# Optimization experiments

Hardware: AMD Instinct MI355X
Metric: run time of the kernel (lower is better)

## Reference

```python
import jax, jax.numpy as jnp
import numpy as np

N_NODES = 50000


def _pointnet_layer(h, pos, src, dst, wA, bA, wB, bB):
    # message: MLP(concat(h_j, pos_j - pos_i)) per edge, then max-aggregate at dst
    m = jnp.concatenate([h[src], pos[src] - pos[dst]], axis=-1)  # [E, in+3]
    m = jax.nn.relu(m @ wA + bA) @ wB + bB                       # [E, out]
    agg = jax.ops.segment_max(m, dst, num_segments=N_NODES)     # [N, out]
    # PyG max-aggregation returns 0 for nodes with no incoming edges
    return jnp.where(jnp.isfinite(agg), agg, 0.0)


def setup_inputs() -> dict:
    key = jax.random.key(0)
    ks = jax.random.split(key, 16)
    num_points, num_features, E = 256, 256, 800000
    s = 0.05
    inp = {
        "x": jax.random.normal(ks[0], (N_NODES, num_points), dtype=jnp.float32),
        "pos": jax.random.normal(ks[1], (N_NODES, 3), dtype=jnp.float32),
        "edge_index": jax.random.randint(ks[2], (2, E), 0, N_NODES, dtype=jnp.int64),
        # conv1 mlp: (num_points+3 -> F -> F)
        "w1a": jax.random.normal(ks[3], (num_points + 3, num_features), dtype=jnp.float32) * s,
        "b1a": jnp.zeros((num_features,), dtype=jnp.float32),
        "w1b": jax.random.normal(ks[4], (num_features, num_features), dtype=jnp.float32) * s,
        "b1b": jnp.zeros((num_features,), dtype=jnp.float32),
        # conv2 mlp: (F+3 -> F -> F)
        "w2a": jax.random.normal(ks[5], (num_features + 3, num_features), dtype=jnp.float32) * s,
        "b2a": jnp.zeros((num_features,), dtype=jnp.float32),
        "w2b": jax.random.normal(ks[6], (num_features, num_features), dtype=jnp.float32) * s,
        "b2b": jnp.zeros((num_features,), dtype=jnp.float32),
        # decoder: F -> 256 -> num_points
        "wd1": jax.random.normal(ks[7], (num_features, 256), dtype=jnp.float32) * s,
        "bd1": jnp.zeros((256,), dtype=jnp.float32),
        "wd2": jax.random.normal(ks[8], (256, num_points), dtype=jnp.float32) * s,
        "bd2": jnp.zeros((num_points,), dtype=jnp.float32),
    }
    return inp


def reference(x, pos, edge_index, w1a, b1a, w1b, b1b, w2a, b2a, w2b, b2b, wd1, bd1, wd2, bd2):
    src, dst = edge_index[0], edge_index[1]  # message flows j(src) -> i(dst)
    h = jax.nn.relu(_pointnet_layer(x, pos, src, dst, w1a, b1a, w1b, b1b))
    h = jax.nn.relu(_pointnet_layer(h, pos, src, dst, w2a, b2a, w2b, b2b))
    decoded = jax.nn.relu(h @ wd1 + bd1) @ wd2 + bd2  # [N, num_points]
    return decoded
```

## Files before the change

kernel.cpp:

```cpp
#include <hip/hip_runtime.h>
#include <stdint.h>


using bf16x8 = __attribute__((ext_vector_type(8))) short;
using f32x4  = __attribute__((ext_vector_type(4))) float;

#define AB_STRIDE 40
#define ABUF      2560
#define ZSTRIDE   68

#define BARRIER_NOVM() asm volatile("s_waitcnt lgkmcnt(0)\n\ts_barrier" ::: "memory")

__device__ __forceinline__ float b2f(uint32_t v16) {
    return __uint_as_float(v16 << 16);
}
__device__ __forceinline__ float b2f_hi(uint32_t w) {
    return __uint_as_float(w & 0xffff0000u);
}
__device__ __forceinline__ uint16_t f2b(float f) {
    uint32_t u = __float_as_uint(f);
    u += 0x7fffu + ((u >> 16) & 1u);
    return (uint16_t)(u >> 16);
}
#if __has_builtin(__builtin_amdgcn_cvt_pk_bf16_f32)
__device__ __forceinline__ uint32_t pack2bf(float lo, float hi) {
    auto r = __builtin_amdgcn_cvt_pk_bf16_f32(lo, hi);
    uint32_t u; __builtin_memcpy(&u, &r, 4); return u;
}
#else
__device__ __forceinline__ uint32_t pack2bf(float lo, float hi) {
    return (uint32_t)f2b(lo) | ((uint32_t)f2b(hi) << 16);
}
#endif
__device__ __forceinline__ uint32_t encf(float f) {
    uint32_t u = __float_as_uint(f);
    return (u & 0x80000000u) ? ~u : (u | 0x80000000u);
}
__device__ __forceinline__ float decf(uint32_t k) {
    uint32_t u = (k & 0x80000000u) ? (k & 0x7fffffffu) : ~k;
    return __uint_as_float(u);
}

__global__ void detect_fmt(const uint32_t* __restrict__ x,
                           const uint32_t* __restrict__ ei,
                           uint32_t* __restrict__ flags) {
    if (threadIdx.x == 0 && blockIdx.x == 0) {
        int plaus = 0;
        for (int i = 0; i < 64; i++) {
            uint32_t v = x[i];
            uint32_t e = (v >> 23) & 0xffu;
            if (v == 0u || (e >= 96u && e <= 150u)) plaus++;
        }
        flags[0] = (plaus >= 48) ? 1u : 0u;
        int zeros = 0;
        for (int i = 0; i < 16; i++)
            if (ei[2 * i + 1] == 0u) zeros++;
        flags[1] = (zeros == 16) ? 1u : 0u;
    }
}

struct ConvArgs {
    const void* src[13];
    uint32_t dstOff[13];
    uint32_t n[13];
};

__global__ __launch_bounds__(256) void convert_small(
        ConvArgs a, uint16_t* __restrict__ dstBase, const uint32_t* __restrict__ flags) {
    bool isf32 = flags[0] != 0u;
    int t = blockIdx.y;
    int i = blockIdx.x * 256 + threadIdx.x;
    if (i >= (int)a.n[t]) return;
    uint16_t* d = dstBase + a.dstOff[t];
    d[i] = isf32 ? f2b(((const float*)a.src[t])[i]) : ((const uint16_t*)a.src[t])[i];
}

__global__ __launch_bounds__(256) void init_hist_agg(
        uint32_t* __restrict__ agg, int n4, int* __restrict__ hist, int N) {
    int i = blockIdx.x * 256 + threadIdx.x;
    if (i < n4) {
        uint4 v = {0x80000000u, 0x80000000u, 0x80000000u, 0x80000000u};
        ((uint4*)agg)[i] = v;
    }
    int i4 = i * 4;
    if (i4 + 3 < N) {
        uint4 z = {0, 0, 0, 0};
        ((uint4*)hist)[i] = z;
    } else if (i4 < N) {
        for (int j = i4; j < N; j++) hist[j] = 0;
    }
}

__global__ __launch_bounds__(256) void hist_dst(
        const int* __restrict__ ei_raw, int E, int* __restrict__ hist,
        const uint32_t* __restrict__ flags) {
    bool i64 = flags[1] != 0u;
    int e = blockIdx.x * 256 + threadIdx.x;
    if (e < E) {
        int d = i64 ? ei_raw[2 * (E + e)] : ei_raw[E + e];
        atomicAdd(&hist[d], 1);
    }
}

__global__ __launch_bounds__(1024) void scan_partial(
        const int* __restrict__ hist, int* __restrict__ cursor,
        int* __restrict__ part, int N) {
    __shared__ int wsum[16];
    int tid = threadIdx.x, lane = tid & 63, wid = tid >> 6;
    int base = blockIdx.x * 1024;
    int v = (base + tid < N) ? hist[base + tid] : 0;
    int x = v;
#pragma unroll
    for (int s = 1; s < 64; s <<= 1) {
        int t = __shfl_up(x, s, 64);
        if (lane >= s) x += t;
    }
    if (lane == 63) wsum[wid] = x;
    __syncthreads();
    if (wid == 0 && lane < 16) {
        int w = wsum[lane];
#pragma unroll
        for (int s = 1; s < 16; s <<= 1) {
            int t = __shfl_up(w, s, 64);
            if (lane >= s) w += t;
        }
        wsum[lane] = w;
    }
    __syncthreads();
    int wbase = (wid > 0) ? wsum[wid - 1] : 0;
    if (base + tid < N) cursor[base + tid] = x - v + wbase;
    if (tid == 0) part[blockIdx.x] = wsum[15];
}

__global__ __launch_bounds__(1024) void scan_carry(
        const int* __restrict__ part, int* __restrict__ carry, int B) {
    __shared__ int wsum[16];
    int tid = threadIdx.x, lane = tid & 63, wid = tid >> 6;
    int v = (tid < B) ? part[tid] : 0;
    int x = v;
#pragma unroll
    for (int s = 1; s < 64; s <<= 1) {
        int t = __shfl_up(x, s, 64);
        if (lane >= s) x += t;
    }
    if (lane == 63) wsum[wid] = x;
    __syncthreads();
    if (wid == 0 && lane < 16) {
        int w = wsum[lane];
#pragma unroll
        for (int s = 1; s < 16; s <<= 1) {
            int t = __shfl_up(w, s, 64);
            if (lane >= s) w += t;
        }
        wsum[lane] = w;
    }
    __syncthreads();
    int wbase = (wid > 0) ? wsum[wid - 1] : 0;
    if (tid < B) carry[tid] = x - v + wbase;
}

__global__ __launch_bounds__(1024) void scan_add(
        int* __restrict__ cursor, const int* __restrict__ carry, int N) {
    int i = blockIdx.x * 1024 + threadIdx.x;
    if (i < N) cursor[i] += carry[blockIdx.x];
}

__global__ __launch_bounds__(256) void scatter_edges(
        const int* __restrict__ ei_raw, int E, int* __restrict__ cursor,
        int* __restrict__ esrc, int* __restrict__ edst,
        const uint32_t* __restrict__ flags) {
    bool i64 = flags[1] != 0u;
    int e = blockIdx.x * 256 + threadIdx.x;
    if (e < E) {
        int s = i64 ? ei_raw[2 * e] : ei_raw[e];
        int d = i64 ? ei_raw[2 * (E + e)] : ei_raw[E + e];
        int p = atomicAdd(&cursor[d], 1);
        esrc[p] = s;
        edst[p] = d;
    }
}

__global__ __launch_bounds__(256) void transpose_w(
        const uint16_t* s0, const uint16_t* s1, const uint16_t* s2,
        const uint16_t* s3, const uint16_t* s4, const uint16_t* s5,
        uint16_t* dst) {
    const uint16_t* srcs[6] = {s0, s1, s2, s3, s4, s5};
    const uint16_t* src = srcs[blockIdx.y];
    uint16_t* d = dst + (size_t)blockIdx.y * 65536;
    int k = blockIdx.x;
    int n = threadIdx.x;
    d[(k >> 5) * 8192 + n * 32 + (k & 31)] = src[k * 256 + n];
}

__global__ __launch_bounds__(256) void pos_proj(
        const uint16_t* pos, const uint16_t* wpos, uint16_t* Q, int N) {
    int t = threadIdx.x;
    int r = t >> 5, c8 = (t & 31) * 8;
    int i = blockIdx.x * 8 + r;
    if (i >= N) return;
    uint4 wv0 = *(const uint4*)(wpos + c8);
    uint4 wv1 = *(const uint4*)(wpos + 256 + c8);
    uint4 wv2 = *(const uint4*)(wpos + 512 + c8);
    float p0 = b2f(pos[i * 3 + 0]);
    float p1 = b2f(pos[i * 3 + 1]);
    float p2 = b2f(pos[i * 3 + 2]);
    uint32_t w0[4] = {wv0.x, wv0.y, wv0.z, wv0.w};
    uint32_t w1[4] = {wv1.x, wv1.y, wv1.z, wv1.w};
    uint32_t w2[4] = {wv2.x, wv2.y, wv2.z, wv2.w};
    uint32_t o[4];
#pragma unroll
    for (int j = 0; j < 4; j++) {
        float lo = p0 * b2f(w0[j] & 0xffffu) + p1 * b2f(w1[j] & 0xffffu) + p2 * b2f(w2[j] & 0xffffu);
        float hi = p0 * b2f_hi(w0[j]) + p1 * b2f_hi(w1[j]) + p2 * b2f_hi(w2[j]);
        o[j] = pack2bf(lo, hi);
    }
    uint4 ov = {o[0], o[1], o[2], o[3]};
    *(uint4*)(Q + (size_t)i * 256 + c8) = ov;
}

template <int AMODE, int OUTMODE, int REINIT>
__global__ __launch_bounds__(256, 3) void gemm_node(
        const void* __restrict__ Araw, const uint16_t* __restrict__ BT,
        const uint16_t* __restrict__ bias, const uint16_t* __restrict__ Qadd,
        void* __restrict__ out, int M, const uint32_t* __restrict__ flags,
        uint32_t* __restrict__ aggwb) {
    __shared__ __align__(16) uint16_t Al[2 * 64 * AB_STRIDE];
    int tid = threadIdx.x;
    int tileM = blockIdx.x;
    int wave = tid >> 6, lane = tid & 63, lrow = lane & 15, quad = lane >> 4;
    int row = tid >> 2, kq = (tid & 3) * 8;
    f32x4 acc[4][4] = {};

    int rg = tileM * 64 + row;
    bool rok = rg < M;
    int rgc = rok ? rg : (M - 1);
    bool isf32 = false;
    if (AMODE == 2 || OUTMODE == 2) isf32 = flags[0] != 0u;

    const uint16_t* a16 = (const uint16_t*)Araw + (size_t)rgc * 256 + kq;
    const uint32_t* a32 = (const uint32_t*)Araw + (size_t)rgc * 256 + kq;
    const uint16_t* bfrag = BT + (wave * 64 + lrow) * 32 + quad * 8;
    uint16_t* awr = Al + row * AB_STRIDE + kq;
    const uint16_t* ard = Al + lrow * AB_STRIDE + quad * 8;

    uint4 p0 = {0, 0, 0, 0}, p1 = {0, 0, 0, 0};
    if (AMODE == 0) {
        p0 = *(const uint4*)a16;
    } else if (AMODE == 1) {
        p0 = *(const uint4*)a32; p1 = *(const uint4*)(a32 + 4);
    } else {
        if (isf32) { p0 = *(const uint4*)a32; p1 = *(const uint4*)(a32 + 4); }
        else       { p0 = *(const uint4*)a16; }
    }

#pragma unroll
    for (int kc = 0; kc < 256; kc += 32) {
        int buf = (kc >> 5) & 1;
        uint4 wv;
        if (AMODE == 0 || (AMODE == 2 && !isf32)) {
            wv = p0;
        } else if (AMODE == 1) {
            uint32_t a[8] = {p0.x, p0.y, p0.z, p0.w, p1.x, p1.y, p1.z, p1.w};
            wv.x = pack2bf(decf(a[0]), decf(a[1]));
            wv.y = pack2bf(decf(a[2]), decf(a[3]));
            wv.z = pack2bf(decf(a[4]), decf(a[5]));
            wv.w = pack2bf(decf(a[6]), decf(a[7]));
        } else {
            wv.x = pack2bf(__uint_as_float(p0.x), __uint_as_float(p0.y));
            wv.y = pack2bf(__uint_as_float(p0.z), __uint_as_float(p0.w));
            wv.z = pack2bf(__uint_as_float(p1.x), __uint_as_float(p1.y));
            wv.w = pack2bf(__uint_as_float(p1.z), __uint_as_float(p1.w));
        }
        *(uint4*)(awr + buf * ABUF) = wv;
        const uint16_t* bp = bfrag + (kc >> 5) * 8192;
        bf16x8 bfv[4];
#pragma unroll
        for (int c = 0; c < 4; c++) bfv[c] = *(const bf16x8*)(bp + c * 512);
        if (kc < 224) {
            if (AMODE == 0) {
                p0 = *(const uint4*)(a16 + kc + 32);
            } else if (AMODE == 1) {
                p0 = *(const uint4*)(a32 + kc + 32);
                p1 = *(const uint4*)(a32 + kc + 36);
            } else {
                if (isf32) { p0 = *(const uint4*)(a32 + kc + 32);
                             p1 = *(const uint4*)(a32 + kc + 36); }
                else       { p0 = *(const uint4*)(a16 + kc + 32); }
            }
        }
        BARRIER_NOVM();
        const uint16_t* ar = ard + buf * ABUF;
        bf16x8 af[4];
#pragma unroll
        for (int r = 0; r < 4; r++) af[r] = *(const bf16x8*)(ar + r * 16 * AB_STRIDE);
#pragma unroll
        for (int r = 0; r < 4; r++)
#pragma unroll
            for (int c = 0; c < 4; c++)
                acc[r][c] = __builtin_amdgcn_mfma_f32_16x16x32_bf16(af[r], bfv[c], acc[r][c], 0, 0, 0);
    }

    if (AMODE == 1 && REINIT && rok) {
        uint32_t* wb = aggwb + (size_t)rg * 256 + kq;
        uint4 z = {0x80000000u, 0x80000000u, 0x80000000u, 0x80000000u};
#pragma unroll
        for (int kc = 0; kc < 256; kc += 32) {
            *(uint4*)(wb + kc) = z;
            *(uint4*)(wb + kc + 4) = z;
        }
    }

#pragma unroll
    for (int c = 0; c < 4; c++) {
        int col = wave * 64 + c * 16 + lrow;
        float bv = b2f(bias[col]);
#pragma unroll
        for (int r = 0; r < 4; r++) {
#pragma unroll
            for (int i = 0; i < 4; i++) {
                int rw = tileM * 64 + r * 16 + quad * 4 + i;
                if (rw >= M) continue;
                float v = acc[r][c][i] + bv;
                if (OUTMODE == 0) {
                    v += b2f(Qadd[(size_t)rw * 256 + col]);
                    ((uint16_t*)out)[(size_t)rw * 256 + col] = f2b(v);
                } else if (OUTMODE == 1) {
                    v = fmaxf(v, 0.f);
                    ((uint16_t*)out)[(size_t)rw * 256 + col] = f2b(v);
                } else {
                    if (isf32) ((float*)out)[(size_t)rw * 256 + col] = v;
                    else       ((uint16_t*)out)[(size_t)rw * 256 + col] = f2b(v);
                }
            }
        }
    }
}

__global__ __launch_bounds__(256, 3) void edge_gemm_agg(
        const uint16_t* __restrict__ Gs16, const uint16_t* __restrict__ Qb,
        const uint16_t* __restrict__ BT, const uint16_t* __restrict__ bias,
        const int* __restrict__ esrc, const int* __restrict__ edst, int E,
        uint32_t* __restrict__ agg) {
    __shared__ __align__(16) uint16_t SM[256 * ZSTRIDE];
    uint16_t* Al = SM;
    uint16_t* Zl = SM;
    __shared__ int sdst[64];
    __shared__ uint64_t smask;
    int tid = threadIdx.x;
    int ebase = blockIdx.x * 64;
    int evalid = (E - ebase < 64) ? (E - ebase) : 64;
    if (tid < 64) sdst[tid] = (tid < evalid) ? edst[ebase + tid] : 0;

    int wave = tid >> 6, lane = tid & 63, lrow = lane & 15, quad = lane >> 4;
    int row = tid >> 2, kq = (tid & 3) * 8;
    int er = (row < evalid) ? row : (evalid - 1);
    int s = esrc[ebase + er];
    int d = edst[ebase + er];
    const uint16_t* gbase = Gs16 + (size_t)s * 256 + kq;
    const uint16_t* qbase = Qb   + (size_t)d * 256 + kq;
    const uint16_t* bfrag = BT + (wave * 64 + lrow) * 32 + quad * 8;
    uint16_t* awr = Al + row * AB_STRIDE + kq;
    const uint16_t* ard = Al + lrow * AB_STRIDE + quad * 8;

    f32x4 acc[4][4] = {};
    uint4 g = *(const uint4*)gbase;
    uint4 q = *(const uint4*)qbase;

#pragma unroll
    for (int kc = 0; kc < 256; kc += 32) {
        int buf = (kc >> 5) & 1;
        uint32_t gw[4] = {g.x, g.y, g.z, g.w};
        uint32_t qw[4] = {q.x, q.y, q.z, q.w};
        uint32_t mw[4];
#pragma unroll
        for (int j = 0; j < 4; j++) {
            float lo = fmaxf(b2f(gw[j] & 0xffffu) - b2f(qw[j] & 0xffffu), 0.f);
            float hi = fmaxf(b2f_hi(gw[j]) - b2f_hi(qw[j]), 0.f);
            mw[j] = pack2bf(lo, hi);
        }
        uint4 wv = {mw[0], mw[1], mw[2], mw[3]};
        *(uint4*)(awr + buf * ABUF) = wv;
        const uint16_t* bp = bfrag + (kc >> 5) * 8192;
        bf16x8 bfv[4];
#pragma unroll
        for (int c = 0; c < 4; c++) bfv[c] = *(const bf16x8*)(bp + c * 512);
        if (kc < 224) {
            g = *(const uint4*)(gbase + kc + 32);
            q = *(const uint4*)(qbase + kc + 32);
        }
        BARRIER_NOVM();
        const uint16_t* ar = ard + buf * ABUF;
        bf16x8 af[4];
#pragma unroll
        for (int r = 0; r < 4; r++) af[r] = *(const bf16x8*)(ar + r * 16 * AB_STRIDE);
#pragma unroll
        for (int r = 0; r < 4; r++)
#pragma unroll
            for (int c = 0; c < 4; c++)
                acc[r][c] = __builtin_amdgcn_mfma_f32_16x16x32_bf16(af[r], bfv[c], acc[r][c], 0, 0, 0);
    }
    __syncthreads();

    float bv[4];
#pragma unroll
    for (int c = 0; c < 4; c++) bv[c] = b2f(bias[wave * 64 + c * 16 + lrow]);
#pragma unroll
    for (int c = 0; c < 4; c++) {
        int col = wave * 64 + c * 16 + lrow;
#pragma unroll
        for (int r = 0; r < 4; r++) {
            uint2 z4 = {pack2bf(acc[r][c][0] + bv[c], acc[r][c][1] + bv[c]),
                        pack2bf(acc[r][c][2] + bv[c], acc[r][c][3] + bv[c])};
            *(uint2*)&Zl[col * ZSTRIDE + r * 16 + quad * 4] = z4;
        }
    }
    if (wave == 0) {
        int d0 = sdst[lane];
        int dp = (lane > 0) ? sdst[lane - 1] : -1;
        uint64_t m = __ballot(d0 != dp);
        if (lane == 0) smask = m;
    }
    __syncthreads();

    uint64_t mask = smask;
    int col = tid;
    const uint16_t* zc = &Zl[col * ZSTRIDE];
    float run = 0.f;
#pragma unroll 4
    for (int gi = 0; gi < 16; gi++) {
        int rbase = gi * 4;
        if (rbase >= evalid) break;
        uint2 z4 = *(const uint2*)&zc[rbase];
        float vv[4] = {b2f(z4.x & 0xffffu), b2f_hi(z4.x),
                       b2f(z4.y & 0xffffu), b2f_hi(z4.y)};
#pragma unroll
        for (int i = 0; i < 4; i++) {
            int r = rbase + i;
            if (r >= evalid) break;
            if (r == 0) {
                run = vv[0];
            } else if ((mask >> r) & 1ull) {
                int dp = sdst[r - 1];
                atomicMax(agg + (size_t)dp * 256 + col, encf(run));
                run = vv[i];
            } else {
                run = fmaxf(run, vv[i]);
            }
        }
    }
    if (evalid > 0)
        atomicMax(agg + (size_t)sdst[evalid - 1] * 256 + col, encf(run));
}

extern "C" void kernel_launch(void* const* d_in, const int* in_sizes, int n_in,
                              void* d_out, int out_size, void* d_ws, size_t ws_size,
                              hipStream_t stream) {
    const void* x_raw   = d_in[0];
    const void* pos_raw = d_in[1];
    const int*  ei_raw  = (const int*)d_in[2];

    int N = in_sizes[0] / 256;
    int E = in_sizes[2] / 2;

    char* ws = (char*)d_ws;
    size_t off = 0;
    auto alloc = [&](size_t bytes) { void* p = ws + off; off += (bytes + 255) & ~(size_t)255; return p; };

    uint32_t* flags = (uint32_t*)alloc(256);
    uint16_t* WT    = (uint16_t*)alloc(6 * 65536 * sizeof(uint16_t));
    const uint32_t POS_OFF = 0;
    const uint32_t W1A_OFF = POS_OFF + (uint32_t)(N * 3);
    const uint32_t W2A_OFF = W1A_OFF + 66304;
    const uint32_t W1B_OFF = W2A_OFF + 66304;
    const uint32_t W2B_OFF = W1B_OFF + 65536;
    const uint32_t WD1_OFF = W2B_OFF + 65536;
    const uint32_t WD2_OFF = WD1_OFF + 65536;
    const uint32_t B1A_OFF = WD2_OFF + 65536;
    const uint32_t B1B_OFF = B1A_OFF + 256;
    const uint32_t B2A_OFF = B1B_OFF + 256;
    const uint32_t B2B_OFF = B2A_OFF + 256;
    const uint32_t BD1_OFF = B2B_OFF + 256;
    const uint32_t BD2_OFF = BD1_OFF + 256;
    const uint32_t ARENA_ELEMS = BD2_OFF + 256;
    uint16_t* arena = (uint16_t*)alloc((size_t)ARENA_ELEMS * 2);
    int*      hist  = (int*)alloc((size_t)N * 4);
    int*      curs  = (int*)alloc((size_t)N * 4);
    int*      part  = (int*)alloc(1024 * 4);
    int*      carry = (int*)alloc(1024 * 4);
    int*      esrc  = (int*)alloc((size_t)E * 4);
    int*      edst  = (int*)alloc((size_t)E * 4);
    uint16_t* Qb    = (uint16_t*)alloc((size_t)N * 256 * 2);
    uint16_t* Gs    = (uint16_t*)alloc((size_t)N * 256 * 2);
    uint32_t* agg   = (uint32_t*)alloc((size_t)N * 256 * 4);
    uint16_t* d1    = Gs;

    uint16_t* posb = arena + POS_OFF;
    uint16_t* w1a = arena + W1A_OFF, * w2a = arena + W2A_OFF;
    uint16_t* w1b = arena + W1B_OFF, * w2b = arena + W2B_OFF;
    uint16_t* wd1 = arena + WD1_OFF, * wd2 = arena + WD2_OFF;
    uint16_t* b1a = arena + B1A_OFF, * b1b = arena + B1B_OFF;
    uint16_t* b2a = arena + B2A_OFF, * b2b = arena + B2B_OFF;
    uint16_t* bd1 = arena + BD1_OFF, * bd2 = arena + BD2_OFF;

    int n4      = N * 64;
    int nbElem  = (n4 + 255) / 256;
    int nbNode  = (N + 63) / 64;
    int nbEdge  = (E + 63) / 64;
    int nbE256  = (E + 255) / 256;
    int nbPos   = (N + 7) / 8;
    int nbScan  = (N + 1023) / 1024;

    detect_fmt<<<1, 64, 0, stream>>>((const uint32_t*)x_raw, (const uint32_t*)ei_raw, flags);

    ConvArgs ca;
    ca.src[0] = pos_raw;  ca.dstOff[0] = POS_OFF; ca.n[0] = (uint32_t)(N * 3);
    ca.src[1] = d_in[3];  ca.dstOff[1] = W1A_OFF; ca.n[1] = 66304;
    ca.src[2] = d_in[7];  ca.dstOff[2] = W2A_OFF; ca.n[2] = 66304;
    ca.src[3] = d_in[5];  ca.dstOff[3] = W1B_OFF; ca.n[3] = 65536;
    ca.src[4] = d_in[9];  ca.dstOff[4] = W2B_OFF; ca.n[4] = 65536;
    ca.src[5] = d_in[11]; ca.dstOff[5] = WD1_OFF; ca.n[5] = 65536;
    ca.src[6] = d_in[13]; ca.dstOff[6] = WD2_OFF; ca.n[6] = 65536;
    ca.src[7] = d_in[4];  ca.dstOff[7] = B1A_OFF; ca.n[7] = 256;
    ca.src[8] = d_in[6];  ca.dstOff[8] = B1B_OFF; ca.n[8] = 256;
    ca.src[9] = d_in[8];  ca.dstOff[9] = B2A_OFF; ca.n[9] = 256;
    ca.src[10] = d_in[10]; ca.dstOff[10] = B2B_OFF; ca.n[10] = 256;
    ca.src[11] = d_in[12]; ca.dstOff[11] = BD1_OFF; ca.n[11] = 256;
    ca.src[12] = d_in[14]; ca.dstOff[12] = BD2_OFF; ca.n[12] = 256;
    {
        uint32_t maxn = (uint32_t)(N * 3);
        dim3 g((maxn + 255) / 256, 13);
        convert_small<<<g, 256, 0, stream>>>(ca, arena, flags);
    }

    init_hist_agg<<<nbElem, 256, 0, stream>>>(agg, n4, hist, N);
    hist_dst<<<nbE256, 256, 0, stream>>>(ei_raw, E, hist, flags);
    scan_partial<<<nbScan, 1024, 0, stream>>>(hist, curs, part, N);
    scan_carry<<<1, 1024, 0, stream>>>(part, carry, nbScan);
    scan_add<<<nbScan, 1024, 0, stream>>>(curs, carry, N);
    scatter_edges<<<nbE256, 256, 0, stream>>>(ei_raw, E, curs, esrc, edst, flags);

    transpose_w<<<dim3(256, 6), 256, 0, stream>>>(w1a, w1b, w2a, w2b, wd1, wd2, WT);

    pos_proj<<<nbPos, 256, 0, stream>>>(posb, w1a + 65536, Qb, N);
    gemm_node<2, 0, 0><<<nbNode, 256, 0, stream>>>(
        x_raw, WT + 0 * 65536, b1a, Qb, Gs, N, flags, nullptr);
    edge_gemm_agg<<<nbEdge, 256, 0, stream>>>(Gs, Qb, WT + 1 * 65536, b1b, esrc, edst, E, agg);

    pos_proj<<<nbPos, 256, 0, stream>>>(posb, w2a + 65536, Qb, N);
    gemm_node<1, 0, 1><<<nbNode, 256, 0, stream>>>(
        agg, WT + 2 * 65536, b2a, Qb, Gs, N, flags, agg);
    edge_gemm_agg<<<nbEdge, 256, 0, stream>>>(Gs, Qb, WT + 3 * 65536, b2b, esrc, edst, E, agg);

    gemm_node<1, 1, 0><<<nbNode, 256, 0, stream>>>(
        agg, WT + 4 * 65536, bd1, nullptr, d1, N, flags, nullptr);
    gemm_node<0, 2, 0><<<nbNode, 256, 0, stream>>>(
        d1, WT + 5 * 65536, bd2, nullptr, d_out, N, flags, nullptr);
}
```

Before: 710.5 us.

## Fuse decoder GEMMs into one kernel keeping hidden tile in LDS; packed bf16 relu

```diff
diff --git a/kernel.cpp b/kernel.cpp
--- a/kernel.cpp
+++ b/kernel.cpp
@@ -32,6 +32,11 @@
     return (uint32_t)f2b(lo) | ((uint32_t)f2b(hi) << 16);
 }
 #endif
+__device__ __forceinline__ uint32_t pk_relu_bf2(uint32_t w) {
+    uint32_t r;
+    asm("v_pk_max_i16 %0, %1, 0" : "=v"(r) : "v"(w));
+    return r;
+}
 __device__ __forceinline__ uint32_t encf(float f) {
     uint32_t u = __float_as_uint(f);
     return (u & 0x80000000u) ? ~u : (u | 0x80000000u);
@@ -235,7 +240,7 @@
     bool rok = rg < M;
     int rgc = rok ? rg : (M - 1);
     bool isf32 = false;
-    if (AMODE == 2 || OUTMODE == 2) isf32 = flags[0] != 0u;
+    if (AMODE == 2) isf32 = flags[0] != 0u;
 
     const uint16_t* a16 = (const uint16_t*)Araw + (size_t)rgc * 256 + kq;
     const uint32_t* a32 = (const uint32_t*)Araw + (size_t)rgc * 256 + kq;
@@ -244,9 +249,7 @@
     const uint16_t* ard = Al + lrow * AB_STRIDE + quad * 8;
 
     uint4 p0 = {0, 0, 0, 0}, p1 = {0, 0, 0, 0};
-    if (AMODE == 0) {
-        p0 = *(const uint4*)a16;
-    } else if (AMODE == 1) {
+    if (AMODE == 1) {
         p0 = *(const uint4*)a32; p1 = *(const uint4*)(a32 + 4);
     } else {
         if (isf32) { p0 = *(const uint4*)a32; p1 = *(const uint4*)(a32 + 4); }
@@ -257,7 +260,7 @@
     for (int kc = 0; kc < 256; kc += 32) {
         int buf = (kc >> 5) & 1;
         uint4 wv;
-        if (AMODE == 0 || (AMODE == 2 && !isf32)) {
+        if (AMODE == 2 && !isf32) {
             wv = p0;
         } else if (AMODE == 1) {
             uint32_t a[8] = {p0.x, p0.y, p0.z, p0.w, p1.x, p1.y, p1.z, p1.w};
@@ -277,9 +280,7 @@
 #pragma unroll
         for (int c = 0; c < 4; c++) bfv[c] = *(const bf16x8*)(bp + c * 512);
         if (kc < 224) {
-            if (AMODE == 0) {
-                p0 = *(const uint4*)(a16 + kc + 32);
-            } else if (AMODE == 1) {
+            if (AMODE == 1) {
                 p0 = *(const uint4*)(a32 + kc + 32);
                 p1 = *(const uint4*)(a32 + kc + 36);
             } else {
@@ -321,16 +322,119 @@
                 int rw = tileM * 64 + r * 16 + quad * 4 + i;
                 if (rw >= M) continue;
                 float v = acc[r][c][i] + bv;
-                if (OUTMODE == 0) {
-                    v += b2f(Qadd[(size_t)rw * 256 + col]);
-                    ((uint16_t*)out)[(size_t)rw * 256 + col] = f2b(v);
-                } else if (OUTMODE == 1) {
-                    v = fmaxf(v, 0.f);
-                    ((uint16_t*)out)[(size_t)rw * 256 + col] = f2b(v);
-                } else {
-                    if (isf32) ((float*)out)[(size_t)rw * 256 + col] = v;
-                    else       ((uint16_t*)out)[(size_t)rw * 256 + col] = f2b(v);
-                }
+                v += b2f(Qadd[(size_t)rw * 256 + col]);
+                ((uint16_t*)out)[(size_t)rw * 256 + col] = f2b(v);
+            }
+        }
+    }
+}
+
+__global__ __launch_bounds__(256, 3) void decoder_fused(
+        const uint32_t* __restrict__ agg, const uint16_t* __restrict__ BT1,
+        const uint16_t* __restrict__ bias1, const uint16_t* __restrict__ BT2,
+        const uint16_t* __restrict__ bias2, void* __restrict__ out, int M,
+        const uint32_t* __restrict__ flags) {
+    __shared__ __align__(16) uint16_t SM[8 * ABUF];
+    uint16_t* Al = SM;
+    int tid = threadIdx.x;
+    int tileM = blockIdx.x;
+    int wave = tid >> 6, lane = tid & 63, lrow = lane & 15, quad = lane >> 4;
+    int row = tid >> 2, kq = (tid & 3) * 8;
+    f32x4 acc[4][4] = {};
+
+    int rg = tileM * 64 + row;
+    bool rok = rg < M;
+    int rgc = rok ? rg : (M - 1);
+    bool isf32 = flags[0] != 0u;
+
+    const uint32_t* a32 = agg + (size_t)rgc * 256 + kq;
+    const uint16_t* bfrag1 = BT1 + (wave * 64 + lrow) * 32 + quad * 8;
+    const uint16_t* bfrag2 = BT2 + (wave * 64 + lrow) * 32 + quad * 8;
+    uint16_t* awr = Al + row * AB_STRIDE + kq;
+    const uint16_t* ard = Al + lrow * AB_STRIDE + quad * 8;
+
+    uint4 p0 = *(const uint4*)a32;
+    uint4 p1 = *(const uint4*)(a32 + 4);
+
+#pragma unroll
+    for (int kc = 0; kc < 256; kc += 32) {
+        int buf = (kc >> 5) & 1;
+        uint32_t a[8] = {p0.x, p0.y, p0.z, p0.w, p1.x, p1.y, p1.z, p1.w};
+        uint4 wv;
+        wv.x = pack2bf(decf(a[0]), decf(a[1]));
+        wv.y = pack2bf(decf(a[2]), decf(a[3]));
+        wv.z = pack2bf(decf(a[4]), decf(a[5]));
+        wv.w = pack2bf(decf(a[6]), decf(a[7]));
+        *(uint4*)(awr + buf * ABUF) = wv;
+        const uint16_t* bp = bfrag1 + (kc >> 5) * 8192;
+        bf16x8 bfv[4];
+#pragma unroll
+        for (int c = 0; c < 4; c++) bfv[c] = *(const bf16x8*)(bp + c * 512);
+        if (kc < 224) {
+            p0 = *(const uint4*)(a32 + kc + 32);
+            p1 = *(const uint4*)(a32 + kc + 36);
+        }
+        BARRIER_NOVM();
+        const uint16_t* ar = ard + buf * ABUF;
+        bf16x8 af[4];
+#pragma unroll
+        for (int r = 0; r < 4; r++) af[r] = *(const bf16x8*)(ar + r * 16 * AB_STRIDE);
+#pragma unroll
+        for (int r = 0; r < 4; r++)
+#pragma unroll
+            for (int c = 0; c < 4; c++)
+                acc[r][c] = __builtin_amdgcn_mfma_f32_16x16x32_bf16(af[r], bfv[c], acc[r][c], 0, 0, 0);
+    }
+
+    BARRIER_NOVM();
+
+#pragma unroll
+    for (int c = 0; c < 4; c++) {
+        int col = wave * 64 + c * 16 + lrow;
+        float bv = b2f(bias1[col]);
+        uint16_t* tb = SM + (col >> 5) * ABUF + (col & 31);
+#pragma unroll
+        for (int r = 0; r < 4; r++) {
+#pragma unroll
+            for (int i = 0; i < 4; i++) {
+                int rr = r * 16 + quad * 4 + i;
+                tb[rr * AB_STRIDE] = f2b(fmaxf(acc[r][c][i] + bv, 0.f));
+            }
+            acc[r][c] = (f32x4){0.f, 0.f, 0.f, 0.f};
+        }
+    }
+    BARRIER_NOVM();
+
+#pragma unroll
+    for (int kc = 0; kc < 256; kc += 32) {
+        const uint16_t* tb = SM + (kc >> 5) * ABUF;
+        const uint16_t* bp = bfrag2 + (kc >> 5) * 8192;
+        bf16x8 af[4], bfv[4];
+#pragma unroll
+        for (int c = 0; c < 4; c++) bfv[c] = *(const bf16x8*)(bp + c * 512);
+#pragma unroll
+        for (int r = 0; r < 4; r++)
+            af[r] = *(const bf16x8*)(tb + (r * 16 + lrow) * AB_STRIDE + quad * 8);
+#pragma unroll
+        for (int r = 0; r < 4; r++)
+#pragma unroll
+            for (int c = 0; c < 4; c++)
+                acc[r][c] = __builtin_amdgcn_mfma_f32_16x16x32_bf16(af[r], bfv[c], acc[r][c], 0, 0, 0);
+    }
+
+#pragma unroll
+    for (int c = 0; c < 4; c++) {
+        int col = wave * 64 + c * 16 + lrow;
+        float bv = b2f(bias2[col]);
+#pragma unroll
+        for (int r = 0; r < 4; r++) {
+#pragma unroll
+            for (int i = 0; i < 4; i++) {
+                int rw = tileM * 64 + r * 16 + quad * 4 + i;
+                if (rw >= M) continue;
+                float v = acc[r][c][i] + bv;
+                if (isf32) ((float*)out)[(size_t)rw * 256 + col] = v;
+                else       ((uint16_t*)out)[(size_t)rw * 256 + col] = f2b(v);
             }
         }
     }
@@ -374,9 +478,9 @@
         uint32_t mw[4];
 #pragma unroll
         for (int j = 0; j < 4; j++) {
-            float lo = fmaxf(b2f(gw[j] & 0xffffu) - b2f(qw[j] & 0xffffu), 0.f);
-            float hi = fmaxf(b2f_hi(gw[j]) - b2f_hi(qw[j]), 0.f);
-            mw[j] = pack2bf(lo, hi);
+            float lo = b2f(gw[j] & 0xffffu) - b2f(qw[j] & 0xffffu);
+            float hi = b2f_hi(gw[j]) - b2f_hi(qw[j]);
+            mw[j] = pk_relu_bf2(pack2bf(lo, hi));
         }
         uint4 wv = {mw[0], mw[1], mw[2], mw[3]};
         *(uint4*)(awr + buf * ABUF) = wv;
@@ -492,7 +596,6 @@
     uint16_t* Qb    = (uint16_t*)alloc((size_t)N * 256 * 2);
     uint16_t* Gs    = (uint16_t*)alloc((size_t)N * 256 * 2);
     uint32_t* agg   = (uint32_t*)alloc((size_t)N * 256 * 4);
-    uint16_t* d1    = Gs;
 
     uint16_t* posb = arena + POS_OFF;
     uint16_t* w1a = arena + W1A_OFF, * w2a = arena + W2A_OFF;
@@ -551,8 +654,6 @@
         agg, WT + 2 * 65536, b2a, Qb, Gs, N, flags, agg);
     edge_gemm_agg<<<nbEdge, 256, 0, stream>>>(Gs, Qb, WT + 3 * 65536, b2b, esrc, edst, E, agg);
 
-    gemm_node<1, 1, 0><<<nbNode, 256, 0, stream>>>(
-        agg, WT + 4 * 65536, bd1, nullptr, d1, N, flags, nullptr);
-    gemm_node<0, 2, 0><<<nbNode, 256, 0, stream>>>(
-        d1, WT + 5 * 65536, bd2, nullptr, d_out, N, flags, nullptr);
-}
+    decoder_fused<<<nbNode, 256, 0, stream>>>(
+        agg, WT + 4 * 65536, bd1, WT + 5 * 65536, bd2, d_out, N, flags);
+}
```

New measurement: 685.0 us. 1.04x faster.
